# Optimization experiments

Measured on AMD Instinct MI355X. Metric: run time of the kernel, lower is better.

Reference implementation:

```python
import jax, jax.numpy as jnp
import numpy as np

D = 1024      # embedding_dim
H = 16        # num_heads
DH = D // H   # head_dim
DFF = 4 * D
EPS = 1e-5


def setup_inputs() -> dict:
    key = jax.random.key(0)
    ks = jax.random.split(key, 10)
    B, T = 2, 2048
    s = 0.02
    return {
        "x": jax.random.normal(ks[0], (B, T, D), dtype=jnp.float32),
        "Wq": jax.random.normal(ks[1], (H, D, DH), dtype=jnp.float32) * s,
        "Wk": jax.random.normal(ks[2], (H, D, DH), dtype=jnp.float32) * s,
        "Wv": jax.random.normal(ks[3], (H, D, DH), dtype=jnp.float32) * s,
        "W1": jax.random.normal(ks[4], (D, DFF), dtype=jnp.float32) * s,
        "b1": jnp.zeros((DFF,), dtype=jnp.float32),
        "W2": jax.random.normal(ks[5], (DFF, D), dtype=jnp.float32) * s,
        "b2": jnp.zeros((D,), dtype=jnp.float32),
        "gamma1": jnp.ones((D,), dtype=jnp.float32),
        "beta1": jnp.zeros((D,), dtype=jnp.float32),
        "gamma2": jnp.ones((D,), dtype=jnp.float32),
        "beta2": jnp.zeros((D,), dtype=jnp.float32),
    }


def _layernorm(x, gamma, beta):
    # torch.var default is unbiased (ddof=1) -- faithful to LayerNorm1d
    mean = jnp.mean(x, axis=-1, keepdims=True)
    var = jnp.var(x, axis=-1, keepdims=True, ddof=1)
    return gamma * (x - mean) * jax.lax.rsqrt(var + EPS) + beta


def _block(x, Wq, Wk, Wv, W1, b1, W2, b2, gamma1, beta1, gamma2, beta2):
    B, T, _ = x.shape
    h = _layernorm(x, gamma1, beta1)
    # per-head projections stacked: [B,H,T,DH]
    Q = jnp.einsum('btd,hde->bhte', h, Wq)
    K = jnp.einsum('btd,hde->bhte', h, Wk)
    V = jnp.einsum('btd,hde->bhte', h, Wv)
    # NOTE: original scales by 1/sqrt(embedding_dim), NOT head_dim
    scores = jnp.einsum('bhqe,bhke->bhqk', Q, K) / jnp.sqrt(jnp.float32(D))
    causal = jnp.tril(jnp.ones((T, T), dtype=bool))
    scores = jnp.where(causal, scores, -jnp.inf)
    attn = jax.nn.softmax(scores, axis=-1)
    out = jnp.einsum('bhqk,bhke->bhqe', attn, V)
    # torch.cat over heads along last dim == transpose+reshape
    out = out.transpose(0, 2, 1, 3).reshape(B, T, D)
    x = x + out
    h2 = _layernorm(x, gamma2, beta2)
    ff = jax.nn.relu(h2 @ W1 + b1) @ W2 + b2  # dropout is identity at inference
    return x + ff


def reference(x, Wq, Wk, Wv, W1, b1, W2, b2, gamma1, beta1, gamma2, beta2):
    return _block(x, Wq, Wk, Wv, W1, b1, W2, b2, gamma1, beta1, gamma2, beta2)
```

## Files before the change

kernel.cpp:

```cpp
#include <hip/hip_runtime.h>

typedef unsigned short u16;
typedef __bf16 bf16;
typedef __attribute__((ext_vector_type(8))) __bf16 bf16x8;
typedef __attribute__((ext_vector_type(4))) float f32x4;
typedef __attribute__((ext_vector_type(8))) unsigned short u16x8;
typedef unsigned long long u64;

__device__ __forceinline__ float bf2f(u16 h) {
  return __uint_as_float(((unsigned int)h) << 16);
}
__device__ __forceinline__ u16 f2bf(float f) {
  unsigned int u = __float_as_uint(f);
  return (u16)((u + 0x7fffu + ((u >> 16) & 1u)) >> 16);
}
__device__ __forceinline__ u16 ld_cv(const void* p, size_t i, int f32) {
  return f32 ? f2bf(((const float*)p)[i]) : ((const u16*)p)[i];
}
__device__ __forceinline__ float ld_f(const void* p, size_t i, int f32) {
  return f32 ? ((const float*)p)[i] : bf2f(((const u16*)p)[i]);
}
__device__ __forceinline__ void async16(const u16* g, u16* l) {
  __builtin_amdgcn_global_load_lds(
      (const __attribute__((address_space(1))) unsigned int*)g,
      (__attribute__((address_space(3))) unsigned int*)l, 16, 0, 0);
}
__device__ __forceinline__ unsigned pk_bf16(float hi, float lo) {
  return __builtin_amdgcn_perm(__float_as_uint(hi) + 0x8000u,
                               __float_as_uint(lo) + 0x8000u, 0x07060302u);
}

__global__ void sniff_kernel(const u16* __restrict__ x, int* __restrict__ flag) {
  const int tid = threadIdx.x;
  int me = 0;
#pragma unroll
  for (int j = 0; j < 4; j++) {
    const u16 v = x[(tid * 4 + j) * 2];
    const int e = (v >> 7) & 0xFF;
    me = me > e ? me : e;
  }
#pragma unroll
  for (int off = 32; off > 0; off >>= 1) {
    const int o = __shfl_down(me, off);
    me = me > o ? me : o;
  }
  __shared__ int sm[4];
  if ((tid & 63) == 0) sm[tid >> 6] = me;
  __syncthreads();
  if (tid == 0) {
    int a = sm[0] > sm[1] ? sm[0] : sm[1];
    int b = sm[2] > sm[3] ? sm[2] : sm[3];
    *flag = ((a > b ? a : b) >= 140) ? 1 : 0;
  }
}

__global__ void prep_kernel(const void* __restrict__ Wq, const void* __restrict__ Wk,
                            const void* __restrict__ Wv, const void* __restrict__ W1,
                            const void* __restrict__ W2,
                            u16* __restrict__ WTq, u16* __restrict__ W1T,
                            u16* __restrict__ W2T, const int* __restrict__ flag) {
  __shared__ u16 tile[64][65];
  const int f = *flag;
  const int bid = blockIdx.x;
  const int lx = threadIdx.x & 63, ly = threadIdx.x >> 6;
  if (bid < 768) {
    const int bx = bid & 15, wh = bid >> 4;
    const int w = wh >> 4, hh = wh & 15;
    const int tr = bx * 64;
    const void* W = (w == 0) ? Wq : ((w == 1) ? Wk : Wv);
    const size_t hbase = (size_t)hh * 65536;
#pragma unroll
    for (int i = 0; i < 16; i++)
      tile[ly * 16 + i][lx] = ld_cv(W, hbase + (size_t)(tr + ly * 16 + i) * 64 + lx, f);
    __syncthreads();
#pragma unroll
    for (int i = 0; i < 16; i++)
      WTq[((size_t)(w * 1024 + hh * 64 + ly * 16 + i)) * 1024 + tr + lx] =
          tile[lx][ly * 16 + i];
  } else {
    const void* src;
    u16* dst;
    int R, C, tc, tr;
    if (bid < 1792) {
      const int j = bid - 768;
      src = W1; dst = W1T; R = 1024; C = 4096;
      tc = (j & 63) * 64; tr = (j >> 6) * 64;
    } else {
      const int j = bid - 1792;
      src = W2; dst = W2T; R = 4096; C = 1024;
      tc = (j & 15) * 64; tr = (j >> 4) * 64;
    }
#pragma unroll
    for (int i = 0; i < 16; i++)
      tile[ly * 16 + i][lx] = ld_cv(src, (size_t)(tr + ly * 16 + i) * C + tc + lx, f);
    __syncthreads();
#pragma unroll
    for (int i = 0; i < 16; i++)
      dst[(size_t)(tc + ly * 16 + i) * R + tr + lx] = tile[lx][ly * 16 + i];
  }
}

template <int EPI, int WR, int WC, bool MS>
__launch_bounds__(WR * WC * 64)
__global__ void gemm_bt(const u16* __restrict__ A, const u16* __restrict__ B,
                        int K, int KLD, int NX, int N,
                        const void* __restrict__ bias, const u16* __restrict__ res,
                        void* __restrict__ out,
                        u16* __restrict__ Qo, u16* __restrict__ Ko, u16* __restrict__ Vto,
                        const int* __restrict__ flag) {
  constexpr int BM = WR * 64, BN = WC * 64, T = WR * WC * 64;
  constexpr int RPA = T / 4;
  constexpr int RAH = BM / RPA;
  constexpr int RBH = BN / RPA;
  __shared__ __align__(16) u16 As[BM * 64];
  __shared__ __align__(16) u16 Bs[BN * 64];
  const int tid = threadIdx.x;
  const int bid = blockIdx.x;
  const int sxp = NX >> 3;
  const int xcd = bid & 7, j9 = bid >> 3;
  int m0, n0, koff = 0, khb = 0;
  if (EPI == 3) {
    m0 = (xcd * 4 + (j9 & 3)) * BM;
    n0 = ((j9 >> 2) & 7) * BN;
    khb = (j9 >> 5) & 1;
    koff = khb * K;
  } else if (MS) {
    m0 = (xcd * sxp + j9 % sxp) * BM;
    n0 = (j9 / sxp) * BN;
  } else {
    n0 = (xcd * sxp + j9 % sxp) * BN;
    m0 = (j9 / sxp) * BM;
  }
  const int wave = tid >> 6, lane = tid & 63;
  const int wm = (wave / WC) * 64, wn = (wave % WC) * 64;
  const int lm = lane & 15, lq = lane >> 4;
  const int fb = (EPI == 1 || EPI == 2) ? *flag : 0;

  const f32x4 zero = {0.f, 0.f, 0.f, 0.f};
  f32x4 acc[4][4];
#pragma unroll
  for (int i = 0; i < 4; i++)
#pragma unroll
    for (int j = 0; j < 4; j++) acc[i][j] = zero;

  const int ar = tid >> 2;
  const int ac = ((tid & 3) ^ ((tid >> 3) & 3)) * 8;
  const u16* Ag = A + (size_t)(m0 + ar) * KLD + koff + ac;
  const u16* Bg = B + (size_t)(n0 + ar) * KLD + koff + ac;
  u16* AsP = &As[tid * 8];
  u16* BsP = &Bs[tid * 8];
  const int rq = (lq ^ ((lm >> 1) & 3)) * 8;

  for (int k0 = 0; k0 < K; k0 += 64) {
#pragma unroll
    for (int hh = 0; hh < 2; hh++) {
#pragma unroll
      for (int c = 0; c < RAH; c++)
        async16(Ag + k0 + hh * 32 + (size_t)c * RPA * KLD,
                AsP + hh * BM * 32 + c * RPA * 32);
#pragma unroll
      for (int c = 0; c < RBH; c++)
        async16(Bg + k0 + hh * 32 + (size_t)c * RPA * KLD,
                BsP + hh * BN * 32 + c * RPA * 32);
    }
    __syncthreads();
    bf16x8 a0[4], a1[4], b0[4], b1[4];
#pragma unroll
    for (int i = 0; i < 4; i++) {
      a0[i] = *(const bf16x8*)&As[(wm + i * 16 + lm) * 32 + rq];
      a1[i] = *(const bf16x8*)&As[BM * 32 + (wm + i * 16 + lm) * 32 + rq];
    }
#pragma unroll
    for (int i = 0; i < 4; i++) {
      b0[i] = *(const bf16x8*)&Bs[(wn + i * 16 + lm) * 32 + rq];
      b1[i] = *(const bf16x8*)&Bs[BN * 32 + (wn + i * 16 + lm) * 32 + rq];
    }
#pragma unroll
    for (int i = 0; i < 4; i++)
#pragma unroll
      for (int j = 0; j < 4; j++) {
        acc[i][j] = __builtin_amdgcn_mfma_f32_16x16x32_bf16(a0[i], b0[j], acc[i][j], 0, 0, 0);
        acc[i][j] = __builtin_amdgcn_mfma_f32_16x16x32_bf16(a1[i], b1[j], acc[i][j], 0, 0, 0);
      }
    __syncthreads();
  }

  if (EPI == 0) {
#pragma unroll
    for (int i = 0; i < 4; i++) {
      const int row0 = m0 + wm + i * 16 + lq * 4;
      const int bb = row0 >> 11, t0 = row0 & 2047;
#pragma unroll
      for (int j = 0; j < 4; j++) {
        const int col = n0 + wn + j * 16 + lm;
        const int w = col >> 10, nn = col & 1023;
        const int hh = nn >> 6, e = nn & 63;
        if (w == 2) {
          ushort4 v4;
          v4.x = f2bf(acc[i][j][0]);
          v4.y = f2bf(acc[i][j][1]);
          v4.z = f2bf(acc[i][j][2]);
          v4.w = f2bf(acc[i][j][3]);
          *(ushort4*)&Vto[(((size_t)(bb * 16 + hh)) * 64 + e) * 2048 + t0] = v4;
        } else {
          u16* dst = (w == 0) ? Qo : Ko;
#pragma unroll
          for (int r = 0; r < 4; r++)
            dst[(((size_t)(bb * 16 + hh)) * 2048 + t0 + r) * 64 + e] =
                f2bf(acc[i][j][r]);
        }
      }
    }
  } else if (EPI == 3) {
    u16* P = khb ? Ko : Qo;
#pragma unroll
    for (int i = 0; i < 4; i++) {
#pragma unroll
      for (int r = 0; r < 4; r++) {
        const int row = m0 + wm + i * 16 + lq * 4 + r;
#pragma unroll
        for (int j = 0; j < 4; j++) {
          const int col = n0 + wn + j * 16 + lm;
          P[(size_t)row * N + col] = f2bf(acc[i][j][r]);
        }
      }
    }
  } else {
#pragma unroll
    for (int i = 0; i < 4; i++) {
#pragma unroll
      for (int r = 0; r < 4; r++) {
        const int row = m0 + wm + i * 16 + lq * 4 + r;
#pragma unroll
        for (int j = 0; j < 4; j++) {
          const int col = n0 + wn + j * 16 + lm;
          const float c = acc[i][j][r];
          if (EPI == 1) {
            const float v = c + ld_f(bias, col, fb);
            ((u16*)out)[(size_t)row * N + col] = f2bf(v > 0.f ? v : 0.f);
          } else {
            const float v = c + ld_f(bias, col, fb) + bf2f(res[(size_t)row * N + col]);
            if (fb)
              ((float*)out)[(size_t)row * N + col] = v;
            else
              ((u16*)out)[(size_t)row * N + col] = f2bf(v);
          }
        }
      }
    }
  }
}

__launch_bounds__(256)
__global__ void ffn2_reduce(const u16* __restrict__ P0, const u16* __restrict__ P1,
                            const void* __restrict__ bias, const u16* __restrict__ res,
                            void* __restrict__ out, const int* __restrict__ flag) {
  const int f = *flag;
  const size_t i0 = ((size_t)blockIdx.x * 256 + threadIdx.x) * 8;
  const int col = (int)(i0 & 1023);
  const u16x8 a8 = *(const u16x8*)(P0 + i0);
  const u16x8 b8 = *(const u16x8*)(P1 + i0);
  const u16x8 r8 = *(const u16x8*)(res + i0);
  float v[8];
#pragma unroll
  for (int k = 0; k < 8; k++)
    v[k] = bf2f(a8[k]) + bf2f(b8[k]) + ld_f(bias, col + k, f) + bf2f(r8[k]);
  if (f) {
    float4 o0 = {v[0], v[1], v[2], v[3]};
    float4 o1 = {v[4], v[5], v[6], v[7]};
    *(float4*)((float*)out + i0) = o0;
    *(float4*)((float*)out + i0 + 4) = o1;
  } else {
    u16x8 o8;
#pragma unroll
    for (int k = 0; k < 8; k++) o8[k] = f2bf(v[k]);
    *(u16x8*)((u16*)out + i0) = o8;
  }
}

__launch_bounds__(256, 2)
__global__ void attn_mfma(const u16* __restrict__ Q, const u16* __restrict__ K,
                          const u16* __restrict__ Vt, const void* __restrict__ xres,
                          const int* __restrict__ flag, u16* __restrict__ x2) {
  __shared__ __align__(16) u16 smem[2][4096];
  const int tid = threadIdx.x;
  const int wave = tid >> 6, lane = tid & 63;
  const int lm = lane & 15, quad = lane >> 4;
  const int bid = blockIdx.x;
  const int bh = (bid & 7) + 8 * ((bid >> 3) & 3);
  const int p = bid >> 5;
  const int b = bh >> 4, h = bh & 15;
  const int f32in = *flag;
  const int qb = (wave < 2) ? (2 * p + wave) : (63 - 2 * p - (wave & 1));
  const int qw0 = qb * 32;
  const int nt = 64 - 2 * p;

  const u16* Kbh = K + (size_t)bh * 131072;
  const u16* Vbh = Vt + (size_t)bh * 131072;
  const f32x4 zero = {0.f, 0.f, 0.f, 0.f};
  const int srow = lane >> 2;
  const int sch2 = ((lane & 3) ^ ((srow >> 1) & 3)) * 8;
  const int rk = (lm >> 1) & 3;

  bf16x8 qf[2][2];
#pragma unroll
  for (int s = 0; s < 2; s++) {
    const u16* Qp = Q + ((size_t)bh * 2048 + qw0 + s * 16 + lm) * 64 + quad * 8;
    qf[s][0] = *(const bf16x8*)Qp;
    qf[s][1] = *(const bf16x8*)(Qp + 32);
  }
  __builtin_amdgcn_s_waitcnt(0x0F70);

  f32x4 ot[2][4];
#pragma unroll
  for (int s = 0; s < 2; s++)
#pragma unroll
    for (int j = 0; j < 4; j++) ot[s][j] = zero;
  float l[2] = {0.f, 0.f};

  union V8 { bf16x8 v; struct { u64 lo, hi; } q; };

  auto stage2 = [&](int t, u16* buf) {
    const int ks = t * 32;
    if (wave < 2) {
#pragma unroll
      for (int c = 0; c < 2; c++)
        async16(Kbh + (size_t)(ks + c * 16 + srow) * 64 + wave * 32 + sch2,
                buf + wave * 1024 + c * 512 + lane * 8);
    } else {
      const int cb = (wave & 1) * 2;
#pragma unroll
      for (int c = cb; c < cb + 2; c++)
        async16(Vbh + (size_t)(c * 16 + srow) * 2048 + ks + sch2,
                buf + 2048 + c * 512 + lane * 8);
    }
  };

  stage2(0, smem[0]);

#pragma unroll 1
  for (int t = 0; t < nt; t++) {
    if (t + 1 < nt) {
      stage2(t + 1, smem[(t + 1) & 1]);
      asm volatile("s_waitcnt vmcnt(2)" ::: "memory");
    } else {
      asm volatile("s_waitcnt vmcnt(0)" ::: "memory");
    }
    __builtin_amdgcn_s_barrier();
    if (t <= qb) {
      const u16* Ksw = smem[t & 1];
      const u16* Vsw = Ksw + 2048;
      bf16x8 kk[2][2];
#pragma unroll
      for (int hh = 0; hh < 2; hh++) {
        kk[hh][0] = *(const bf16x8*)&Ksw[(hh * 16 + lm) * 32 + (quad ^ rk) * 8];
        kk[hh][1] = *(const bf16x8*)&Ksw[1024 + (hh * 16 + lm) * 32 + (quad ^ rk) * 8];
      }
      V8 vf[4];
#pragma unroll
      for (int j = 0; j < 4; j++) {
        vf[j].q.lo = *(const u64*)&Vsw[(j * 16 + lm) * 32 +
                                       (((quad >> 1)) ^ rk) * 8 + (quad & 1) * 4];
        vf[j].q.hi = *(const u64*)&Vsw[(j * 16 + lm) * 32 +
                                       (((quad >> 1) | 2) ^ rk) * 8 + (quad & 1) * 4];
      }
      f32x4 S[2][2];
      __builtin_amdgcn_s_setprio(1);
#pragma unroll
      for (int s = 0; s < 2; s++)
#pragma unroll
        for (int hh = 0; hh < 2; hh++) {
          f32x4 a = zero;
          a = __builtin_amdgcn_mfma_f32_16x16x32_bf16(kk[hh][0], qf[s][0], a, 0, 0, 0);
          a = __builtin_amdgcn_mfma_f32_16x16x32_bf16(kk[hh][1], qf[s][1], a, 0, 0, 0);
          S[s][hh] = a;
        }
      __builtin_amdgcn_s_setprio(0);
      const bool maskT = (t == qb);
#pragma unroll
      for (int s = 0; s < 2; s++) {
        float pv[2][4];
#pragma unroll
        for (int hh = 0; hh < 2; hh++)
#pragma unroll
          for (int r = 0; r < 4; r++) {
            float v = __expf(S[s][hh][r] * 0.03125f);
            if (maskT && (hh * 16 + quad * 4 + r > s * 16 + lm)) v = 0.f;
            l[s] += v;
            pv[hh][r] = v;
          }
        unsigned pk[4];
        pk[0] = pk_bf16(pv[0][1], pv[0][0]);
        pk[1] = pk_bf16(pv[0][3], pv[0][2]);
        pk[2] = pk_bf16(pv[1][1], pv[1][0]);
        pk[3] = pk_bf16(pv[1][3], pv[1][2]);
        const bf16x8 pf = *(const bf16x8*)pk;
        __builtin_amdgcn_s_setprio(1);
#pragma unroll
        for (int j = 0; j < 4; j++)
          ot[s][j] = __builtin_amdgcn_mfma_f32_16x16x32_bf16(vf[j].v, pf, ot[s][j], 0, 0, 0);
        __builtin_amdgcn_s_setprio(0);
      }
    }
    __builtin_amdgcn_s_barrier();
  }

#pragma unroll
  for (int s = 0; s < 2; s++) {
    l[s] += __shfl_xor(l[s], 16);
    l[s] += __shfl_xor(l[s], 32);
  }
#pragma unroll
  for (int s = 0; s < 2; s++) {
    const float linv = 1.f / l[s];
    const int row = qw0 + s * 16 + lm;
    const size_t rb = ((size_t)(b * 2048 + row)) * 1024 + h * 64 + quad * 4;
#pragma unroll
    for (int j = 0; j < 4; j++) {
      float xv[4];
      if (f32in) {
        const float4 u = *(const float4*)((const float*)xres + rb + j * 16);
        xv[0] = u.x; xv[1] = u.y; xv[2] = u.z; xv[3] = u.w;
      } else {
        const ushort4 u = *(const ushort4*)((const u16*)xres + rb + j * 16);
        xv[0] = bf2f(u.x); xv[1] = bf2f(u.y); xv[2] = bf2f(u.z); xv[3] = bf2f(u.w);
      }
      ushort4 o;
      o.x = f2bf(xv[0] + ot[s][j][0] * linv);
      o.y = f2bf(xv[1] + ot[s][j][1] * linv);
      o.z = f2bf(xv[2] + ot[s][j][2] * linv);
      o.w = f2bf(xv[3] + ot[s][j][3] * linv);
      *(ushort4*)&x2[rb + j * 16] = o;
    }
  }
}

__launch_bounds__(256)
__global__ void ln_kernel(const void* __restrict__ x, const void* __restrict__ gamma,
                          const void* __restrict__ beta, u16* __restrict__ out,
                          const int* __restrict__ flag, int xraw) {
  const size_t row = blockIdx.x;
  const int tid = threadIdx.x;
  const int f = *flag;
  const int fx = xraw ? f : 0;
  float v0, v1, v2, v3;
  if (fx) {
    const float4 v = *((const float4*)x + row * 256 + tid);
    v0 = v.x; v1 = v.y; v2 = v.z; v3 = v.w;
  } else {
    const ushort4 u = *((const ushort4*)x + row * 256 + tid);
    v0 = bf2f(u.x); v1 = bf2f(u.y); v2 = bf2f(u.z); v3 = bf2f(u.w);
  }
  float s = v0 + v1 + v2 + v3;
  float sq = v0 * v0 + v1 * v1 + v2 * v2 + v3 * v3;
#pragma unroll
  for (int off = 32; off > 0; off >>= 1) {
    s += __shfl_down(s, off);
    sq += __shfl_down(sq, off);
  }
  __shared__ float ss[4], ssq[4];
  if ((tid & 63) == 0) { ss[tid >> 6] = s; ssq[tid >> 6] = sq; }
  __syncthreads();
  s = ss[0] + ss[1] + ss[2] + ss[3];
  sq = ssq[0] + ssq[1] + ssq[2] + ssq[3];
  const float mean = s * (1.f / 1024.f);
  const float var = (sq - 1024.f * mean * mean) * (1.f / 1023.f);
  const float rs = rsqrtf(var + 1e-5f);
  const int c0 = tid * 4;
  ushort4 o;
  o.x = f2bf(ld_f(gamma, c0 + 0, f) * (v0 - mean) * rs + ld_f(beta, c0 + 0, f));
  o.y = f2bf(ld_f(gamma, c0 + 1, f) * (v1 - mean) * rs + ld_f(beta, c0 + 1, f));
  o.z = f2bf(ld_f(gamma, c0 + 2, f) * (v2 - mean) * rs + ld_f(beta, c0 + 2, f));
  o.w = f2bf(ld_f(gamma, c0 + 3, f) * (v3 - mean) * rs + ld_f(beta, c0 + 3, f));
  *(ushort4*)&out[row * 1024 + tid * 4] = o;
}

extern "C" void kernel_launch(void* const* d_in, const int* in_sizes, int n_in,
                              void* d_out, int out_size, void* d_ws, size_t ws_size,
                              hipStream_t stream) {
  const void* x      = d_in[0];
  const void* Wq     = d_in[1];
  const void* Wk     = d_in[2];
  const void* Wv     = d_in[3];
  const void* W1     = d_in[4];
  const void* b1     = d_in[5];
  const void* W2     = d_in[6];
  const void* b2     = d_in[7];
  const void* gamma1 = d_in[8];
  const void* beta1  = d_in[9];
  const void* gamma2 = d_in[10];
  const void* beta2  = d_in[11];
  u16* ws = (u16*)d_ws;

  const size_t M4 = 4194304;
  u16* h   = ws;
  u16* Qb  = ws + 1 * M4;
  u16* Kb  = ws + 2 * M4;
  u16* Vtb = ws + 3 * M4;
  u16* WTq = ws + 4 * M4;
  u16* x2  = ws + 4 * M4;
  u16* h2  = ws + 5 * M4;
  u16* W1T = ws + 6 * M4;
  u16* W2T = ws + 7 * M4;
  u16* ff1 = ws;
  u16* P0  = ws + 5 * M4;
  u16* P1  = ws + 6 * M4;
  int* flag = (int*)(ws + 8 * M4 + 9216);

  sniff_kernel<<<1, 256, 0, stream>>>((const u16*)x, flag);
  prep_kernel<<<2816, 256, 0, stream>>>(Wq, Wk, Wv, W1, W2, WTq, W1T, W2T, flag);
  ln_kernel<<<4096, 256, 0, stream>>>(x, gamma1, beta1, h, flag, 1);
  gemm_bt<0, 4, 2, false><<<384, 512, 0, stream>>>(h, WTq, 1024, 1024, 24, 3072,
                                                   nullptr, nullptr, nullptr,
                                                   Qb, Kb, Vtb, flag);
  attn_mfma<<<512, 256, 0, stream>>>(Qb, Kb, Vtb, x, flag, x2);
  ln_kernel<<<4096, 256, 0, stream>>>(x2, gamma2, beta2, h2, flag, 0);
  gemm_bt<1, 4, 2, false><<<512, 512, 0, stream>>>(h2, W1T, 1024, 1024, 32, 4096,
                                                   b1, nullptr, ff1,
                                                   nullptr, nullptr, nullptr, flag);
  gemm_bt<3, 2, 2, false><<<512, 256, 0, stream>>>(ff1, W2T, 2048, 4096, 8, 1024,
                                                   nullptr, nullptr, nullptr,
                                                   P0, P1, nullptr, flag);
  ffn2_reduce<<<2048, 256, 0, stream>>>(P0, P1, b2, x2, d_out, flag);
}
```

Before: 324.5 us.

## Split causal attention into single-wave blocks of 64 query rows without barriers

The attention kernel changes from 256-thread blocks, where four waves share K/V tiles staged in LDS and pair light and heavy query blocks, to 64-thread blocks. In the new version one wave loads its own K/V tiles and handles 64 query rows. Blocks are ordered heaviest first, and the diagonal masking is generalised to cover the last two key tiles. Removing the block barriers and the cross-wave coupling is meant to let waves run independently and schedule more flexibly. In exchange, K/V loads are no longer shared across waves, so global and LDS traffic per query row goes up, and each wave holds more registers.

New measurement: 360.6 us. +11.1%, slower.

```diff
diff --git a/kernel.cpp b/kernel.cpp
--- a/kernel.cpp
+++ b/kernel.cpp
@@ -278,22 +278,20 @@
   }
 }
 
-__launch_bounds__(256, 2)
+__launch_bounds__(64)
 __global__ void attn_mfma(const u16* __restrict__ Q, const u16* __restrict__ K,
                           const u16* __restrict__ Vt, const void* __restrict__ xres,
                           const int* __restrict__ flag, u16* __restrict__ x2) {
   __shared__ __align__(16) u16 smem[2][4096];
-  const int tid = threadIdx.x;
-  const int wave = tid >> 6, lane = tid & 63;
+  const int lane = threadIdx.x;
   const int lm = lane & 15, quad = lane >> 4;
   const int bid = blockIdx.x;
   const int bh = (bid & 7) + 8 * ((bid >> 3) & 3);
-  const int p = bid >> 5;
+  const int q64 = 31 - (bid >> 5);
   const int b = bh >> 4, h = bh & 15;
   const int f32in = *flag;
-  const int qb = (wave < 2) ? (2 * p + wave) : (63 - 2 * p - (wave & 1));
-  const int qw0 = qb * 32;
-  const int nt = 64 - 2 * p;
+  const int qw0 = q64 * 64;
+  const int nt = 2 * q64 + 2;
 
   const u16* Kbh = K + (size_t)bh * 131072;
   const u16* Vbh = Vt + (size_t)bh * 131072;
@@ -302,116 +300,118 @@
   const int sch2 = ((lane & 3) ^ ((srow >> 1) & 3)) * 8;
   const int rk = (lm >> 1) & 3;
 
-  bf16x8 qf[2][2];
-#pragma unroll
-  for (int s = 0; s < 2; s++) {
+  bf16x8 qf[4][2];
+#pragma unroll
+  for (int s = 0; s < 4; s++) {
     const u16* Qp = Q + ((size_t)bh * 2048 + qw0 + s * 16 + lm) * 64 + quad * 8;
     qf[s][0] = *(const bf16x8*)Qp;
     qf[s][1] = *(const bf16x8*)(Qp + 32);
   }
   __builtin_amdgcn_s_waitcnt(0x0F70);
 
-  f32x4 ot[2][4];
-#pragma unroll
-  for (int s = 0; s < 2; s++)
+  f32x4 ot[4][4];
+#pragma unroll
+  for (int s = 0; s < 4; s++)
 #pragma unroll
     for (int j = 0; j < 4; j++) ot[s][j] = zero;
-  float l[2] = {0.f, 0.f};
+  float l[4] = {0.f, 0.f, 0.f, 0.f};
 
   union V8 { bf16x8 v; struct { u64 lo, hi; } q; };
 
-  auto stage2 = [&](int t, u16* buf) {
+  auto stageKV = [&](int t, u16* buf) {
     const int ks = t * 32;
-    if (wave < 2) {
+#pragma unroll
+    for (int hh2 = 0; hh2 < 2; hh2++)
 #pragma unroll
       for (int c = 0; c < 2; c++)
-        async16(Kbh + (size_t)(ks + c * 16 + srow) * 64 + wave * 32 + sch2,
-                buf + wave * 1024 + c * 512 + lane * 8);
-    } else {
-      const int cb = (wave & 1) * 2;
-#pragma unroll
-      for (int c = cb; c < cb + 2; c++)
-        async16(Vbh + (size_t)(c * 16 + srow) * 2048 + ks + sch2,
-                buf + 2048 + c * 512 + lane * 8);
-    }
+        async16(Kbh + (size_t)(ks + c * 16 + srow) * 64 + hh2 * 32 + sch2,
+                buf + hh2 * 1024 + c * 512 + lane * 8);
+#pragma unroll
+    for (int c = 0; c < 4; c++)
+      async16(Vbh + (size_t)(c * 16 + srow) * 2048 + ks + sch2,
+              buf + 2048 + c * 512 + lane * 8);
   };
 
-  stage2(0, smem[0]);
+  stageKV(0, smem[0]);
 
 #pragma unroll 1
   for (int t = 0; t < nt; t++) {
     if (t + 1 < nt) {
-      stage2(t + 1, smem[(t + 1) & 1]);
-      asm volatile("s_waitcnt vmcnt(2)" ::: "memory");
+      stageKV(t + 1, smem[(t + 1) & 1]);
+      asm volatile("s_waitcnt vmcnt(8)" ::: "memory");
     } else {
       asm volatile("s_waitcnt vmcnt(0)" ::: "memory");
     }
-    __builtin_amdgcn_s_barrier();
-    if (t <= qb) {
-      const u16* Ksw = smem[t & 1];
-      const u16* Vsw = Ksw + 2048;
-      bf16x8 kk[2][2];
+    const u16* Ksw = smem[t & 1];
+    const u16* Vsw = Ksw + 2048;
+    bf16x8 kk[2][2];
+#pragma unroll
+    for (int hh = 0; hh < 2; hh++) {
+      kk[hh][0] = *(const bf16x8*)&Ksw[(hh * 16 + lm) * 32 + (quad ^ rk) * 8];
+      kk[hh][1] = *(const bf16x8*)&Ksw[1024 + (hh * 16 + lm) * 32 + (quad ^ rk) * 8];
+    }
+    V8 vf[4];
+#pragma unroll
+    for (int j = 0; j < 4; j++) {
+      vf[j].q.lo = *(const u64*)&Vsw[(j * 16 + lm) * 32 +
+                                     (((quad >> 1)) ^ rk) * 8 + (quad & 1) * 4];
+      vf[j].q.hi = *(const u64*)&Vsw[(j * 16 + lm) * 32 +
+                                     (((quad >> 1) | 2) ^ rk) * 8 + (quad & 1) * 4];
+    }
+    f32x4 S[4][2];
+    __builtin_amdgcn_s_setprio(1);
+#pragma unroll
+    for (int s = 0; s < 4; s++)
 #pragma unroll
       for (int hh = 0; hh < 2; hh++) {
-        kk[hh][0] = *(const bf16x8*)&Ksw[(hh * 16 + lm) * 32 + (quad ^ rk) * 8];
-        kk[hh][1] = *(const bf16x8*)&Ksw[1024 + (hh * 16 + lm) * 32 + (quad ^ rk) * 8];
-      }
-      V8 vf[4];
-#pragma unroll
-      for (int j = 0; j < 4; j++) {
-        vf[j].q.lo = *(const u64*)&Vsw[(j * 16 + lm) * 32 +
-                                       (((quad >> 1)) ^ rk) * 8 + (quad & 1) * 4];
-        vf[j].q.hi = *(const u64*)&Vsw[(j * 16 + lm) * 32 +
-                                       (((quad >> 1) | 2) ^ rk) * 8 + (quad & 1) * 4];
-      }
-      f32x4 S[2][2];
+        f32x4 a = zero;
+        a = __builtin_amdgcn_mfma_f32_16x16x32_bf16(kk[hh][0], qf[s][0], a, 0, 0, 0);
+        a = __builtin_amdgcn_mfma_f32_16x16x32_bf16(kk[hh][1], qf[s][1], a, 0, 0, 0);
+        S[s][hh] = a;
+      }
+    __builtin_amdgcn_s_setprio(0);
+    const bool maskT = (t >= 2 * q64);
+    const int cb = t * 32 - qw0;
+#pragma unroll
+    for (int s = 0; s < 4; s++) {
+      float pv[2][4];
+#pragma unroll
+      for (int hh = 0; hh < 2; hh++)
+#pragma unroll
+        for (int r = 0; r < 4; r++)
+          pv[hh][r] = __expf(S[s][hh][r] * 0.03125f);
+      if (maskT) {
+#pragma unroll
+        for (int hh = 0; hh < 2; hh++)
+#pragma unroll
+          for (int r = 0; r < 4; r++)
+            if (cb + hh * 16 + quad * 4 + r > s * 16 + lm) pv[hh][r] = 0.f;
+      }
+#pragma unroll
+      for (int hh = 0; hh < 2; hh++)
+#pragma unroll
+        for (int r = 0; r < 4; r++) l[s] += pv[hh][r];
+      unsigned pk[4];
+      pk[0] = pk_bf16(pv[0][1], pv[0][0]);
+      pk[1] = pk_bf16(pv[0][3], pv[0][2]);
+      pk[2] = pk_bf16(pv[1][1], pv[1][0]);
+      pk[3] = pk_bf16(pv[1][3], pv[1][2]);
+      const bf16x8 pf = *(const bf16x8*)pk;
       __builtin_amdgcn_s_setprio(1);
 #pragma unroll
-      for (int s = 0; s < 2; s++)
-#pragma unroll
-        for (int hh = 0; hh < 2; hh++) {
-          f32x4 a = zero;
-          a = __builtin_amdgcn_mfma_f32_16x16x32_bf16(kk[hh][0], qf[s][0], a, 0, 0, 0);
-          a = __builtin_amdgcn_mfma_f32_16x16x32_bf16(kk[hh][1], qf[s][1], a, 0, 0, 0);
-          S[s][hh] = a;
-        }
+      for (int j = 0; j < 4; j++)
+        ot[s][j] = __builtin_amdgcn_mfma_f32_16x16x32_bf16(vf[j].v, pf, ot[s][j], 0, 0, 0);
       __builtin_amdgcn_s_setprio(0);
-      const bool maskT = (t == qb);
-#pragma unroll
-      for (int s = 0; s < 2; s++) {
-        float pv[2][4];
-#pragma unroll
-        for (int hh = 0; hh < 2; hh++)
-#pragma unroll
-          for (int r = 0; r < 4; r++) {
-            float v = __expf(S[s][hh][r] * 0.03125f);
-            if (maskT && (hh * 16 + quad * 4 + r > s * 16 + lm)) v = 0.f;
-            l[s] += v;
-            pv[hh][r] = v;
-          }
-        unsigned pk[4];
-        pk[0] = pk_bf16(pv[0][1], pv[0][0]);
-        pk[1] = pk_bf16(pv[0][3], pv[0][2]);
-        pk[2] = pk_bf16(pv[1][1], pv[1][0]);
-        pk[3] = pk_bf16(pv[1][3], pv[1][2]);
-        const bf16x8 pf = *(const bf16x8*)pk;
-        __builtin_amdgcn_s_setprio(1);
-#pragma unroll
-        for (int j = 0; j < 4; j++)
-          ot[s][j] = __builtin_amdgcn_mfma_f32_16x16x32_bf16(vf[j].v, pf, ot[s][j], 0, 0, 0);
-        __builtin_amdgcn_s_setprio(0);
-      }
-    }
-    __builtin_amdgcn_s_barrier();
-  }
-
-#pragma unroll
-  for (int s = 0; s < 2; s++) {
+    }
+  }
+
+#pragma unroll
+  for (int s = 0; s < 4; s++) {
     l[s] += __shfl_xor(l[s], 16);
     l[s] += __shfl_xor(l[s], 32);
   }
 #pragma unroll
-  for (int s = 0; s < 2; s++) {
+  for (int s = 0; s < 4; s++) {
     const float linv = 1.f / l[s];
     const int row = qw0 + s * 16 + lm;
     const size_t rb = ((size_t)(b * 2048 + row)) * 1024 + h * 64 + quad * 4;
@@ -513,7 +513,7 @@
   gemm_bt<0, 4, 2, false><<<384, 512, 0, stream>>>(h, WTq, 1024, 1024, 24, 3072,
                                                    nullptr, nullptr, nullptr,
                                                    Qb, Kb, Vtb, flag);
-  attn_mfma<<<512, 256, 0, stream>>>(Qb, Kb, Vtb, x, flag, x2);
+  attn_mfma<<<1024, 64, 0, stream>>>(Qb, Kb, Vtb, x, flag, x2);
   ln_kernel<<<4096, 256, 0, stream>>>(x2, gamma2, beta2, h2, flag, 0);
   gemm_bt<1, 4, 2, false><<<512, 512, 0, stream>>>(h2, W1T, 1024, 1024, 32, 4096,
                                                    b1, nullptr, ff1,
```
